# Kernel tuning notes

Measured on AMD Instinct MI355X. Metric: run time of the kernel, lower is better.

Reference implementation:

```python
import jax, jax.numpy as jnp
import numpy as np

SCORE_THR = 0.01
IOU_THR = 0.1          # NOTE: original layer hardcodes 0.1 in tf.image.non_max_suppression
MAX_DET = 100
NEG = jnp.float32(-1e30)


def _iou_one_vs_all(box, boxes):
    # box: [4] (y1,x1,y2,x2), boxes: [N,4]
    y1 = jnp.maximum(box[0], boxes[:, 0])
    x1 = jnp.maximum(box[1], boxes[:, 1])
    y2 = jnp.minimum(box[2], boxes[:, 2])
    x2 = jnp.minimum(box[3], boxes[:, 3])
    inter = jnp.maximum(y2 - y1, 0.0) * jnp.maximum(x2 - x1, 0.0)
    a = (box[2] - box[0]) * (box[3] - box[1])
    b = (boxes[:, 2] - boxes[:, 0]) * (boxes[:, 3] - boxes[:, 1])
    return inter / (a + b - inter + 1e-8)


def _nms_keep(boxes, scores):
    # Greedy NMS as a keep-mask over N anchors. Matches tf.image.non_max_suppression
    # restricted to anchors with score > SCORE_THR, up to MAX_DET selections.
    s = jnp.where(scores > SCORE_THR, scores, NEG)
    keep0 = jnp.zeros(s.shape, dtype=bool)

    def step(carry, _):
        s, keep = carry
        i = jnp.argmax(s)
        ok = s[i] > NEG * 0.5
        keep = keep.at[i].set(ok)
        iou = _iou_one_vs_all(boxes[i], boxes)
        s = jnp.where((iou > IOU_THR) & ok, NEG, s)
        s = s.at[i].set(NEG)
        return (s, keep), None

    (_, keep), _ = jax.lax.scan(step, (s, keep0), None, length=MAX_DET)
    return keep


def _filter_image(boxes_i, cls_i):
    # boxes_i: [N,4], cls_i: [N,C]
    C = cls_i.shape[1]
    # class-specific NMS: keep mask per class -> [C, N]
    keep = jax.vmap(lambda s: _nms_keep(boxes_i, s))(cls_i.T)
    keep_flat = keep.T.reshape(-1)          # [N*C], (anchor, class) flat order
    flat = cls_i.reshape(-1)                # [N*C]
    masked = jnp.where(keep_flat, flat, NEG)
    vals, idx = jax.lax.top_k(masked, MAX_DET)
    valid = vals > NEG * 0.5
    anchor = idx // C
    label = idx % C
    scores_out = jnp.where(valid, jnp.take(flat, idx), -1.0)
    boxes_out = jnp.where(valid[:, None], boxes_i[anchor], -1.0)
    labels_out = jnp.where(valid, label, -1).astype(jnp.int32)
    return boxes_out, scores_out, labels_out


def setup_inputs() -> dict:
    key = jax.random.key(0)
    k1, k2, k3 = jax.random.split(key, 3)
    B, N, C = 4, 49104, 90
    yx1 = jax.random.uniform(k1, (B, N, 2), dtype=jnp.float32) * 512.0
    hw = jax.random.uniform(k2, (B, N, 2), dtype=jnp.float32) * 128.0 + 1.0
    boxes = jnp.concatenate([yx1, yx1 + hw], axis=-1)          # [B,N,4] y1x1y2x2
    classification = jax.random.uniform(k3, (B, N, C), dtype=jnp.float32)
    return {"boxes": boxes, "classification": classification}


def reference(boxes, classification):
    return jax.vmap(_filter_image)(boxes, classification)
```

## Files before the change

kernel.cpp:

```cpp
#include <hip/hip_runtime.h>
#include <stdint.h>

typedef unsigned long long u64;

#define B_ 4
#define N_ 49104
#define C_ 90
#define NCLS (B_ * C_)
#define MAXK 100
#define THR 0.01f
#define CHK 512
#define NB2 2048
#define ACH 128
#define NCH ((N_ + ACH - 1) / ACH)
#define CAPC 32
#define NBIN_M 1280
#define BINBASE 0x3F6E0000u
#define BINSH_M 10

__device__ __forceinline__ float area_of(float y1, float x1, float y2, float x2) {
#pragma clang fp contract(off)
  return (y2 - y1) * (x2 - x1);
}

__device__ __forceinline__ bool iou_gt(float ay1, float ax1, float ay2, float ax2, float aa,
                                       float by1, float bx1, float by2, float bx2, float ba) {
#pragma clang fp contract(off)
  float y1 = fmaxf(ay1, by1);
  float x1 = fmaxf(ax1, bx1);
  float y2 = fminf(ay2, by2);
  float x2 = fminf(ax2, bx2);
  float inter = fmaxf(y2 - y1, 0.0f) * fmaxf(x2 - x1, 0.0f);
  float denom = aa + ba - inter + 1e-8f;
  return (inter / denom) > 0.1f;
}

__device__ __forceinline__ u64 umax64(u64 a, u64 b) { return a > b ? a : b; }

__device__ __forceinline__ u64 shfl_xor_u64(u64 v, int m) {
  int lo = __shfl_xor((int)(unsigned)v, m);
  int hi = __shfl_xor((int)(unsigned)(v >> 32), m);
  return ((u64)(unsigned)hi << 32) | (u64)(unsigned)lo;
}

__device__ __forceinline__ int key2bin_m(u64 k) {
  int d = (int)((unsigned)(k >> 32) - BINBASE);
  int bin = d >> BINSH_M;
  if (d < 0) bin = 0;
  if (bin > NBIN_M - 1) bin = NBIN_M - 1;
  return bin;
}

__global__ __launch_bounds__(256) void select_kernel(const float* __restrict__ cls,
                                                     u64* __restrict__ keybuf,
                                                     unsigned* __restrict__ cnt,
                                                     int capsel, float t0) {
  __shared__ u64 ll[C_ * CAPC];
  __shared__ unsigned lcnt[C_];
  __shared__ unsigned base_s[C_];
  int blk = blockIdx.x;
  int b = blk / NCH, ch = blk - b * NCH;
  int a0 = ch * ACH;
  int aEnd = a0 + ACH; if (aEnd > N_) aEnd = N_;
  int e0 = a0 * C_;
  int nelem = (aEnd - a0) * C_;
  int tid = threadIdx.x;

  for (int i = tid; i < C_; i += 256) lcnt[i] = 0u;
  __syncthreads();

  const float4* src4 = (const float4*)(cls + (size_t)b * N_ * C_ + e0);
  int n4 = nelem >> 2;
  for (int i4 = tid; i4 < n4; i4 += 256) {
    float4 v = src4[i4];
#pragma unroll
    for (int j = 0; j < 4; ++j) {
      float s = (&v.x)[j];
      if (s > t0) {
        int e = e0 + i4 * 4 + j;
        unsigned n = (unsigned)e / (unsigned)C_;
        unsigned c = (unsigned)e - n * (unsigned)C_;
        u64 key = ((u64)__float_as_uint(s) << 32) | (u64)(0xFFFFFFFFu - n);
        unsigned pos = atomicAdd(&lcnt[c], 1u);
        if (pos < CAPC) {
          ll[c * CAPC + pos] = key;
        } else {
          unsigned g = (unsigned)(b * C_) + c;
          unsigned gp = atomicAdd(&cnt[g * 16], 1u);
          if (gp < (unsigned)capsel) keybuf[(size_t)g * capsel + gp] = key;
        }
      }
    }
  }
  __syncthreads();

  if (tid < C_) {
    unsigned cc = lcnt[tid]; if (cc > CAPC) cc = CAPC;
    base_s[tid] = atomicAdd(&cnt[(b * C_ + tid) * 16], cc);
  }
  __syncthreads();

  for (int i = tid; i < C_ * CAPC; i += 256) {
    int c = i >> 5, j = i & 31;
    unsigned cc = lcnt[c]; if (cc > CAPC) cc = CAPC;
    if ((unsigned)j < cc) {
      unsigned pos = base_s[c] + (unsigned)j;
      if (pos < (unsigned)capsel)
        keybuf[(size_t)(b * C_ + c) * capsel + pos] = ll[i];
    }
  }
}

__global__ __launch_bounds__(256) void nms_kernel(const float* __restrict__ boxes,
                                                  const float* __restrict__ cls,
                                                  const u64* __restrict__ keybuf,
                                                  const unsigned* __restrict__ cnt,
                                                  int capsel, float t0,
                                                  u64* __restrict__ keepkeys,
                                                  int* __restrict__ nk_arr) {
  int gcls = blockIdx.x;
  int b = gcls / C_, c = gcls - b * C_;
  __shared__ u64 karr[4096];
  __shared__ unsigned hist[NB2];
  __shared__ u64 ck[CHK];
  __shared__ float4 ckbox[CHK];
  __shared__ float carea[CHK];
  __shared__ float4 kb[MAXK];
  __shared__ float ka[MAXK];
  __shared__ u64 red[256];
  __shared__ int sh_blo, sh_run, sh_nk, sh_cc, sh_over;
  int tid = threadIdx.x;
  int lane = tid & 63;

  for (int i = tid; i < MAXK; i += 256) keepkeys[(size_t)gcls * MAXK + i] = 0ull;
  for (int i = tid; i < NB2; i += 256) hist[i] = 0u;
  if (tid == 0) { sh_nk = 0; sh_over = 0; }
  __syncthreads();

  unsigned Mraw = cnt[gcls * 16];
  bool overflow = (Mraw > (unsigned)capsel);
  int M = overflow ? 0 : (int)Mraw;

  const u64* src = keybuf + (size_t)gcls * capsel;
  for (int i = tid; i < M; i += 256) {
    u64 k = src[i];
    karr[i] = k;
    atomicAdd(&hist[(unsigned)(k >> 44) & (NB2 - 1)], 1u);
  }
  __syncthreads();

  const float4* bx4 = (const float4*)(boxes + (size_t)b * N_ * 4);
  int nk = 0;
  int bhi = NB2, ext = 0;

  while (ext < M && sh_nk < MAXK) {
    if (tid == 0) {
      int rem = M - ext, run = 0, bb = bhi;
      while (bb > 0) {
        unsigned h = hist[bb - 1];
        if (run + (int)h > CHK) break;
        run += (int)h; --bb;
        if (run >= 480 || run >= rem) break;
      }
      if (run == 0) sh_over = 1;
      sh_blo = bb; sh_run = run; sh_cc = 0;
    }
    __syncthreads();
    if (sh_over) break;
    int blo = sh_blo, run = sh_run;

    for (int i = tid; i < M; i += 256) {
      u64 k = karr[i];
      int bin = (int)((unsigned)(k >> 44) & (NB2 - 1));
      if (bin >= blo && bin < bhi) { int p = atomicAdd(&sh_cc, 1); ck[p] = k; }
    }
    for (int i = run + tid; i < CHK; i += 256) ck[i] = 0ull;
    __syncthreads();

    for (int kk2 = 2; kk2 <= CHK; kk2 <<= 1) {
      for (int j = kk2 >> 1; j > 0; j >>= 1) {
        if (tid < CHK / 2) {
          int i1 = 2 * tid - (tid & (j - 1));
          int i2 = i1 | j;
          u64 a = ck[i1], bb2 = ck[i2];
          bool desc = ((i1 & kk2) == 0);
          bool sw = desc ? (a < bb2) : (a > bb2);
          if (sw) { ck[i1] = bb2; ck[i2] = a; }
        }
        __syncthreads();
      }
    }

    for (int i = tid; i < run; i += 256) {
      float4 bxv = bx4[0xFFFFFFFFu - (unsigned)(ck[i] & 0xFFFFFFFFull)];
      ckbox[i] = bxv;
      carea[i] = area_of(bxv.x, bxv.y, bxv.z, bxv.w);
    }
    for (int i = run + tid; i < CHK; i += 256) {
      ckbox[i] = make_float4(0.f, 0.f, 0.f, 0.f);
      carea[i] = 0.f;
    }
    __syncthreads();

    if (tid < 64) {
      float4 cb_[8]; float ca_[8];
#pragma unroll
      for (int s = 0; s < 8; ++s) { cb_[s] = ckbox[s * 64 + lane]; ca_[s] = carea[s * 64 + lane]; }
      u64 alive[8];
#pragma unroll
      for (int s = 0; s < 8; ++s) {
        int lo = s * 64;
        alive[s] = (run >= lo + 64) ? ~0ull
                 : (run > lo ? ((1ull << (run - lo)) - 1ull) : 0ull);
      }
      for (int j = 0; j < nk; ++j) {
        float4 sb = kb[j]; float sa = ka[j];
#pragma unroll
        for (int s = 0; s < 8; ++s)
          alive[s] &= ~__ballot(iou_gt(sb.x, sb.y, sb.z, sb.w, sa,
                                       cb_[s].x, cb_[s].y, cb_[s].z, cb_[s].w, ca_[s]));
      }
#pragma unroll 1
      for (int w = 0; w < 8; ++w) {
        while (alive[w] != 0ull && nk < MAXK) {
          int bit = __ffsll((long long)alive[w]) - 1;
          int i = w * 64 + bit;
          float4 sb = ckbox[i];
          float sa = carea[i];
          u64 key = ck[i];
          if (lane == 0) {
            unsigned anchor = 0xFFFFFFFFu - (unsigned)(key & 0xFFFFFFFFull);
            unsigned flat = anchor * C_ + (unsigned)c;
            keepkeys[(size_t)gcls * MAXK + nk] =
                (key & 0xFFFFFFFF00000000ull) | (u64)(0xFFFFFFFFu - flat);
            kb[nk] = sb; ka[nk] = sa;
          }
          ++nk;
#pragma unroll
          for (int s = 0; s < 8; ++s)
            alive[s] &= ~__ballot(iou_gt(sb.x, sb.y, sb.z, sb.w, sa,
                                         cb_[s].x, cb_[s].y, cb_[s].z, cb_[s].w, ca_[s]));
        }
        if (nk >= MAXK) break;
      }
      if (lane == 0) sh_nk = nk;
    }
    __syncthreads();
    ext += run;
    bhi = blo;
  }

  int nkF = sh_nk;
  if (nkF < MAXK) {
    float teff;
    if (overflow)     teff = 2.0f;
    else if (sh_over) teff = __uint_as_float(0x3F000000u | (((unsigned)bhi << 12) - 1u));
    else              teff = t0;
    const float* sbase = cls + (size_t)b * N_ * C_ + c;
    const float* bx = boxes + (size_t)b * N_ * 4;
    u64* kkp = keepkeys + (size_t)gcls * MAXK;
    int nk2 = nkF;
    while (nk2 < MAXK) {
      u64 best = 0ull;
      for (int n = tid; n < N_; n += 256) {
        float s = sbase[(size_t)n * C_];
        if (s > THR && s <= teff) {
          float y1 = bx[(size_t)n * 4 + 0], x1 = bx[(size_t)n * 4 + 1];
          float y2 = bx[(size_t)n * 4 + 2], x2 = bx[(size_t)n * 4 + 3];
          float ar = area_of(y1, x1, y2, x2);
          bool ov = false;
          for (int j = 0; j < nk2; ++j) {
            float4 kbj = kb[j];
            if (iou_gt(kbj.x, kbj.y, kbj.z, kbj.w, ka[j], y1, x1, y2, x2, ar)) { ov = true; break; }
          }
          if (!ov) {
            u64 key = ((u64)__float_as_uint(s) << 32) | (u64)(0xFFFFFFFFu - (unsigned)n);
            best = umax64(best, key);
          }
        }
      }
      red[tid] = best;
      __syncthreads();
      for (int sft = 128; sft > 0; sft >>= 1) {
        if (tid < sft) red[tid] = umax64(red[tid], red[tid + sft]);
        __syncthreads();
      }
      u64 sel = red[0];
      __syncthreads();
      if (sel == 0ull) {
        if (tid == 0) {
          unsigned target = 0xFFFFFFFFu - (unsigned)c;
          for (int j = 0; j < nk2; ++j)
            if ((unsigned)(kkp[j] & 0xFFFFFFFFull) == target) kkp[j] = 0ull;
        }
        break;
      }
      unsigned anchor = 0xFFFFFFFFu - (unsigned)(sel & 0xFFFFFFFFull);
      if (tid == 0) {
        float y1 = bx[(size_t)anchor * 4 + 0], x1 = bx[(size_t)anchor * 4 + 1];
        float y2 = bx[(size_t)anchor * 4 + 2], x2 = bx[(size_t)anchor * 4 + 3];
        kb[nk2] = make_float4(y1, x1, y2, x2);
        ka[nk2] = area_of(y1, x1, y2, x2);
        unsigned flat = anchor * C_ + (unsigned)c;
        kkp[nk2] = (sel & 0xFFFFFFFF00000000ull) | (u64)(0xFFFFFFFFu - flat);
      }
      ++nk2;
      __syncthreads();
    }
    nkF = nk2;
  }
  if (tid == 0) nk_arr[gcls] = nkF;
}

__global__ __launch_bounds__(256) void merge_kernel(const float* __restrict__ boxes,
                                                    const u64* __restrict__ keepkeys,
                                                    const int* __restrict__ nk_arr,
                                                    float* __restrict__ out) {
  int b = blockIdx.x;
  int tid = threadIdx.x;
  int lane = tid & 63;
  int wid = tid >> 6;
  __shared__ unsigned hist[NBIN_M];
  __shared__ unsigned sfx[NBIN_M];
  __shared__ unsigned wsum[4];
  __shared__ u64 mk[512];
  __shared__ u64 selk[MAXK];
  __shared__ int sh_thr;
  __shared__ unsigned sh_cc;
  const u64* kk = keepkeys + (size_t)b * C_ * MAXK;
  const int TOT = C_ * MAXK;

  for (int i = tid; i < NBIN_M; i += 256) hist[i] = 0u;
  if (tid == 0) { sh_thr = -1; sh_cc = 0u; }
  __syncthreads();
  for (int i = tid; i < TOT; i += 256) {
    u64 k = kk[i];
    if (k != 0ull) atomicAdd(&hist[key2bin_m(k)], 1u);
  }
  __syncthreads();

  const int W = 5;
  int j0 = tid * W;
  unsigned psum = 0;
#pragma unroll
  for (int q = 0; q < W; ++q) {
    int bin = NBIN_M - 1 - (j0 + q);
    if (bin >= 0) psum += hist[bin];
  }
  unsigned incl = psum;
#pragma unroll
  for (int s = 1; s < 64; s <<= 1) {
    unsigned v = (unsigned)__shfl_up((int)incl, s);
    if (lane >= s) incl += v;
  }
  if (lane == 63) wsum[wid] = incl;
  __syncthreads();
  unsigned base = 0;
  for (int w2 = 0; w2 < wid; ++w2) base += wsum[w2];
  unsigned running = base + incl - psum;
  int mythr = -1;
#pragma unroll
  for (int q = 0; q < W; ++q) {
    int bin = NBIN_M - 1 - (j0 + q);
    if (bin >= 0) {
      running += hist[bin];
      sfx[bin] = running;
      if (mythr < 0 && running >= (unsigned)MAXK) mythr = bin;
    }
  }
  if (mythr >= 0) atomicMax(&sh_thr, mythr);
  __syncthreads();

  int thr = sh_thr; if (thr < 0) thr = 0;
  unsigned S = sfx[thr];

  if (S <= 512u) {
    for (int i = tid; i < TOT; i += 256) {
      u64 k = kk[i];
      if (k != 0ull && key2bin_m(k) >= thr) {
        unsigned pos = atomicAdd(&sh_cc, 1u);
        mk[pos] = k;
      }
    }
    __syncthreads();
    for (int i = (int)S + tid; i < 512; i += 256) mk[i] = 0ull;
    __syncthreads();
    for (int k2 = 2; k2 <= 512; k2 <<= 1) {
      for (int j = k2 >> 1; j > 0; j >>= 1) {
        int i1 = 2 * tid - (tid & (j - 1));
        int i2 = i1 | j;
        u64 a = mk[i1], bb2 = mk[i2];
        bool desc = ((i1 & k2) == 0);
        bool sw = desc ? (a < bb2) : (a > bb2);
        if (sw) { mk[i1] = bb2; mk[i2] = a; }
        __syncthreads();
      }
    }
    for (int r = tid; r < MAXK; r += 256) selk[r] = mk[r];
    __syncthreads();
  } else {
    if (wid == 0) {
      int c0 = lane, c1 = lane + 64;
      int len0 = (c0 < C_) ? nk_arr[b * C_ + c0] : 0;
      int len1 = (c1 < C_) ? nk_arr[b * C_ + c1] : 0;
      int h0 = 0, h1 = 0;
      auto fetchc = [&](int cc, int& h, int len) -> u64 {
        while (h < len) {
          u64 k = kk[(size_t)cc * MAXK + h];
          if (k != 0ull) return k;
          ++h;
        }
        return 0ull;
      };
      u64 cand0 = (c0 < C_) ? fetchc(c0, h0, len0) : 0ull;
      u64 cand1 = (c1 < C_) ? fetchc(c1, h1, len1) : 0ull;
      for (int r = 0; r < MAXK; ++r) {
        u64 my = umax64(cand0, cand1);
        u64 g = my;
#pragma unroll
        for (int m = 1; m < 64; m <<= 1) g = umax64(g, shfl_xor_u64(g, m));
        if (lane == 0) selk[r] = g;
        if (g != 0ull && my == g) {
          if (cand0 == g) { ++h0; cand0 = fetchc(c0, h0, len0); }
          else            { ++h1; cand1 = fetchc(c1, h1, len1); }
        }
      }
    }
    __syncthreads();
  }

  for (int r = tid; r < MAXK; r += 256) {
    u64 s = selk[r];
    float oy1, ox1, oy2, ox2, sc, lb;
    if (s != 0ull) {
      unsigned flat = 0xFFFFFFFFu - (unsigned)(s & 0xFFFFFFFFull);
      unsigned anchor = flat / C_;
      unsigned label = flat - anchor * C_;
      sc = __uint_as_float((unsigned)(s >> 32));
      const float4 bp = ((const float4*)(boxes + (size_t)b * N_ * 4))[anchor];
      oy1 = bp.x; ox1 = bp.y; oy2 = bp.z; ox2 = bp.w;
      lb = (float)label;
    } else {
      oy1 = ox1 = oy2 = ox2 = -1.0f; sc = -1.0f; lb = -1.0f;
    }
    float* bo = out + ((size_t)b * MAXK + r) * 4;
    bo[0] = oy1; bo[1] = ox1; bo[2] = oy2; bo[3] = ox2;
    out[(size_t)B_ * MAXK * 4 + b * MAXK + r] = sc;
    out[(size_t)B_ * MAXK * 4 + B_ * MAXK + b * MAXK + r] = lb;
  }
}

extern "C" void kernel_launch(void* const* d_in, const int* in_sizes, int n_in,
                              void* d_out, int out_size, void* d_ws, size_t ws_size,
                              hipStream_t stream) {
  const float* boxes = (const float*)d_in[0];
  const float* cls = (const float*)d_in[1];
  char* ws = (char*)d_ws;

  int capsel; float t0;
  auto need_for = [](int cap) -> size_t {
    return 23040 + (size_t)NCLS * cap * 8 + 288000 + 1440;
  };
  if (ws_size >= need_for(4096))      { capsel = 4096; t0 = 0.93f;  }
  else if (ws_size >= need_for(2048)) { capsel = 2048; t0 = 0.962f; }
  else                                { capsel = 1024; t0 = 0.985f; }

  unsigned* cnt = (unsigned*)ws;
  u64* keybuf = (u64*)(ws + 23040);
  size_t off = 23040 + (size_t)NCLS * capsel * 8;
  u64* keepkeys = (u64*)(ws + off);      off += 288000;
  int* nk_arr = (int*)(ws + off);

  hipMemsetAsync(cnt, 0, 23040, stream);
  select_kernel<<<B_ * NCH, 256, 0, stream>>>(cls, keybuf, cnt, capsel, t0);
  nms_kernel<<<NCLS, 256, 0, stream>>>(boxes, cls, keybuf, cnt, capsel, t0,
                                       keepkeys, nk_arr);
  merge_kernel<<<B_, 256, 0, stream>>>(boxes, keepkeys, nk_arr, (float*)d_out);
}
```

Before: 209.7 us.

## Bucket keys by histogram suffix sums and replace bitonic chunk sort with rank sort

Builds a block-wide suffix-sum scan over the score histogram and scatters keys into bin-ordered positions in shared memory, so each chunk is a contiguous range. Chunk boundaries are found in parallel from the suffix sums instead of a serial thread-0 walk. The bitonic sort becomes a counting-rank sort within the chunk, and box loads are merged into that step. The greedy NMS wave now processes one 64-wide segment at a time and prefetches the next candidate. This trades many barriers and serial work for an O(run^2) rank loop per thread and an extra histogram pass.

```diff
diff --git a/kernel.cpp b/kernel.cpp
--- a/kernel.cpp
+++ b/kernel.cpp
@@ -122,15 +122,18 @@
   int b = gcls / C_, c = gcls - b * C_;
   __shared__ u64 karr[4096];
   __shared__ unsigned hist[NB2];
+  __shared__ unsigned sfx[NB2];
   __shared__ u64 ck[CHK];
   __shared__ float4 ckbox[CHK];
   __shared__ float carea[CHK];
   __shared__ float4 kb[MAXK];
   __shared__ float ka[MAXK];
   __shared__ u64 red[256];
-  __shared__ int sh_blo, sh_run, sh_nk, sh_cc, sh_over;
+  __shared__ unsigned wsum[4];
+  __shared__ int sh_blo, sh_run, sh_nk, sh_over, sh_b1;
   int tid = threadIdx.x;
   int lane = tid & 63;
+  int wid = tid >> 6;
 
   for (int i = tid; i < MAXK; i += 256) keepkeys[(size_t)gcls * MAXK + i] = 0ull;
   for (int i = tid; i < NB2; i += 256) hist[i] = 0u;
@@ -142,10 +145,41 @@
   int M = overflow ? 0 : (int)Mraw;
 
   const u64* src = keybuf + (size_t)gcls * capsel;
+
+  for (int i = tid; i < M; i += 256)
+    atomicAdd(&hist[(unsigned)(src[i] >> 44) & (NB2 - 1)], 1u);
+  __syncthreads();
+
+  {
+    const int W = NB2 / 256;
+    unsigned loc[W];
+    unsigned psum = 0;
+#pragma unroll
+    for (int q = 0; q < W; ++q) {
+      psum += hist[NB2 - 1 - (tid * W + q)];
+      loc[q] = psum;
+    }
+    unsigned incl = psum;
+#pragma unroll
+    for (int s = 1; s < 64; s <<= 1) {
+      unsigned v = (unsigned)__shfl_up((int)incl, s);
+      if (lane >= s) incl += v;
+    }
+    if (lane == 63) wsum[wid] = incl;
+    __syncthreads();
+    unsigned base = incl - psum;
+    for (int w2 = 0; w2 < wid; ++w2) base += wsum[w2];
+#pragma unroll
+    for (int q = 0; q < W; ++q)
+      sfx[NB2 - 1 - (tid * W + q)] = base + loc[q];
+  }
+  __syncthreads();
+
   for (int i = tid; i < M; i += 256) {
     u64 k = src[i];
-    karr[i] = k;
-    atomicAdd(&hist[(unsigned)(k >> 44) & (NB2 - 1)], 1u);
+    unsigned bin = (unsigned)(k >> 44) & (NB2 - 1);
+    unsigned old = atomicSub(&hist[bin], 1u);
+    karr[sfx[bin] - old] = k;
   }
   __syncthreads();
 
@@ -154,94 +188,104 @@
   int bhi = NB2, ext = 0;
 
   while (ext < M && sh_nk < MAXK) {
+    if (tid == 0) sh_b1 = -1;
+    __syncthreads();
+    int rem = M - ext;
+    int target = rem < 480 ? rem : 480;
+    {
+      const int W = NB2 / 256;
+      int mymax = -1;
+#pragma unroll
+      for (int q = 0; q < W; ++q) {
+        int bb = tid * W + q;
+        if (bb < bhi && (int)sfx[bb] >= ext + target) mymax = bb > mymax ? bb : mymax;
+      }
+      if (mymax >= 0) atomicMax(&sh_b1, mymax);
+    }
+    __syncthreads();
     if (tid == 0) {
-      int rem = M - ext, run = 0, bb = bhi;
-      while (bb > 0) {
-        unsigned h = hist[bb - 1];
-        if (run + (int)h > CHK) break;
-        run += (int)h; --bb;
-        if (run >= 480 || run >= rem) break;
+      int b1 = sh_b1;
+      int run = (int)sfx[b1] - ext;
+      int blo = b1;
+      if (run > CHK) {
+        blo = b1 + 1;
+        run = (blo >= NB2) ? 0 : ((int)sfx[blo] - ext);
       }
       if (run == 0) sh_over = 1;
-      sh_blo = bb; sh_run = run; sh_cc = 0;
+      sh_blo = blo; sh_run = run;
     }
     __syncthreads();
     if (sh_over) break;
     int blo = sh_blo, run = sh_run;
 
-    for (int i = tid; i < M; i += 256) {
-      u64 k = karr[i];
-      int bin = (int)((unsigned)(k >> 44) & (NB2 - 1));
-      if (bin >= blo && bin < bhi) { int p = atomicAdd(&sh_cc, 1); ck[p] = k; }
-    }
-    for (int i = run + tid; i < CHK; i += 256) ck[i] = 0ull;
-    __syncthreads();
-
-    for (int kk2 = 2; kk2 <= CHK; kk2 <<= 1) {
-      for (int j = kk2 >> 1; j > 0; j >>= 1) {
-        if (tid < CHK / 2) {
-          int i1 = 2 * tid - (tid & (j - 1));
-          int i2 = i1 | j;
-          u64 a = ck[i1], bb2 = ck[i2];
-          bool desc = ((i1 & kk2) == 0);
-          bool sw = desc ? (a < bb2) : (a > bb2);
-          if (sw) { ck[i1] = bb2; ck[i2] = a; }
-        }
-        __syncthreads();
-      }
-    }
-
-    for (int i = tid; i < run; i += 256) {
-      float4 bxv = bx4[0xFFFFFFFFu - (unsigned)(ck[i] & 0xFFFFFFFFull)];
-      ckbox[i] = bxv;
-      carea[i] = area_of(bxv.x, bxv.y, bxv.z, bxv.w);
-    }
-    for (int i = run + tid; i < CHK; i += 256) {
-      ckbox[i] = make_float4(0.f, 0.f, 0.f, 0.f);
-      carea[i] = 0.f;
+    {
+      u64 k0 = 0ull, k1 = 0ull;
+      if (tid < run) k0 = karr[ext + tid];
+      if (tid + 256 < run) k1 = karr[ext + tid + 256];
+      float4 b0v, b1v;
+      if (tid < run) b0v = bx4[0xFFFFFFFFu - (unsigned)(k0 & 0xFFFFFFFFull)];
+      if (tid + 256 < run) b1v = bx4[0xFFFFFFFFu - (unsigned)(k1 & 0xFFFFFFFFull)];
+      int r0 = 0, r1 = 0;
+      for (int j = 0; j < run; ++j) {
+        u64 kj = karr[ext + j];
+        r0 += (kj > k0);
+        r1 += (kj > k1);
+      }
+      if (tid < run) {
+        ck[r0] = k0; ckbox[r0] = b0v;
+        carea[r0] = area_of(b0v.x, b0v.y, b0v.z, b0v.w);
+      }
+      if (tid + 256 < run) {
+        ck[r1] = k1; ckbox[r1] = b1v;
+        carea[r1] = area_of(b1v.x, b1v.y, b1v.z, b1v.w);
+      }
+      for (int i = run + tid; i < CHK; i += 256) {
+        ck[i] = 0ull;
+        ckbox[i] = make_float4(0.f, 0.f, 0.f, 0.f);
+        carea[i] = 0.f;
+      }
     }
     __syncthreads();
 
     if (tid < 64) {
-      float4 cb_[8]; float ca_[8];
-#pragma unroll
-      for (int s = 0; s < 8; ++s) { cb_[s] = ckbox[s * 64 + lane]; ca_[s] = carea[s * 64 + lane]; }
-      u64 alive[8];
-#pragma unroll
-      for (int s = 0; s < 8; ++s) {
-        int lo = s * 64;
-        alive[s] = (run >= lo + 64) ? ~0ull
-                 : (run > lo ? ((1ull << (run - lo)) - 1ull) : 0ull);
-      }
-      for (int j = 0; j < nk; ++j) {
-        float4 sb = kb[j]; float sa = ka[j];
-#pragma unroll
-        for (int s = 0; s < 8; ++s)
-          alive[s] &= ~__ballot(iou_gt(sb.x, sb.y, sb.z, sb.w, sa,
-                                       cb_[s].x, cb_[s].y, cb_[s].z, cb_[s].w, ca_[s]));
-      }
-#pragma unroll 1
-      for (int w = 0; w < 8; ++w) {
-        while (alive[w] != 0ull && nk < MAXK) {
-          int bit = __ffsll((long long)alive[w]) - 1;
-          int i = w * 64 + bit;
-          float4 sb = ckbox[i];
-          float sa = carea[i];
-          u64 key = ck[i];
-          if (lane == 0) {
-            unsigned anchor = 0xFFFFFFFFu - (unsigned)(key & 0xFFFFFFFFull);
-            unsigned flat = anchor * C_ + (unsigned)c;
-            keepkeys[(size_t)gcls * MAXK + nk] =
-                (key & 0xFFFFFFFF00000000ull) | (u64)(0xFFFFFFFFu - flat);
-            kb[nk] = sb; ka[nk] = sa;
+      int nseg = (run + 63) >> 6;
+      for (int w = 0; w < nseg && nk < MAXK; ++w) {
+        int lo = w << 6;
+        float4 cb = ckbox[lo + lane];
+        float ca = carea[lo + lane];
+        u64 alive = (run >= lo + 64) ? ~0ull : ((1ull << (run - lo)) - 1ull);
+        for (int j = 0; j < nk; ++j) {
+          float4 sb = kb[j]; float sa = ka[j];
+          alive &= ~__ballot(iou_gt(sb.x, sb.y, sb.z, sb.w, sa,
+                                    cb.x, cb.y, cb.z, cb.w, ca));
+        }
+        if (alive != 0ull) {
+          int bit = __ffsll((long long)alive) - 1;
+          float4 sb = ckbox[lo + bit];
+          float sa = carea[lo + bit];
+          u64 key = ck[lo + bit];
+          while (nk < MAXK) {
+            u64 rest = alive & (~1ull << bit);
+            int nbit = __ffsll((long long)rest) - 1;
+            int pi = lo + (nbit >= 0 ? nbit : 0);
+            float4 pb = ckbox[pi]; float pa = carea[pi]; u64 pk = ck[pi];
+            if (lane == 0) {
+              unsigned anchor = 0xFFFFFFFFu - (unsigned)(key & 0xFFFFFFFFull);
+              unsigned flat = anchor * C_ + (unsigned)c;
+              keepkeys[(size_t)gcls * MAXK + nk] =
+                  (key & 0xFFFFFFFF00000000ull) | (u64)(0xFFFFFFFFu - flat);
+              kb[nk] = sb; ka[nk] = sa;
+            }
+            ++nk;
+            alive &= ~__ballot(iou_gt(sb.x, sb.y, sb.z, sb.w, sa,
+                                      cb.x, cb.y, cb.z, cb.w, ca));
+            if (alive == 0ull) break;
+            int newbit = __ffsll((long long)alive) - 1;
+            if (newbit == nbit) { sb = pb; sa = pa; key = pk; }
+            else { sb = ckbox[lo + newbit]; sa = carea[lo + newbit]; key = ck[lo + newbit]; }
+            bit = newbit;
           }
-          ++nk;
-#pragma unroll
-          for (int s = 0; s < 8; ++s)
-            alive[s] &= ~__ballot(iou_gt(sb.x, sb.y, sb.z, sb.w, sa,
-                                         cb_[s].x, cb_[s].y, cb_[s].z, cb_[s].w, ca_[s]));
-        }
-        if (nk >= MAXK) break;
+        }
       }
       if (lane == 0) sh_nk = nk;
     }
@@ -289,9 +333,9 @@
       __syncthreads();
       if (sel == 0ull) {
         if (tid == 0) {
-          unsigned target = 0xFFFFFFFFu - (unsigned)c;
+          unsigned target2 = 0xFFFFFFFFu - (unsigned)c;
           for (int j = 0; j < nk2; ++j)
-            if ((unsigned)(kkp[j] & 0xFFFFFFFFull) == target) kkp[j] = 0ull;
+            if ((unsigned)(kkp[j] & 0xFFFFFFFFull) == target2) kkp[j] = 0ull;
         }
         break;
       }
```

Result: slower. 230.2 us (+9.8%).
